# Performance work log

Hardware: AMD Instinct MI355X
Metric: run time of the kernel (lower is better)

Reference implementation:

```python
import jax, jax.numpy as jnp
import numpy as np
from jax import lax

IMG_W, IMG_H = 800.0, 320.0
NPTS = 72
N_STRIPS = NPTS - 1
MAX_LANES = 4
NUM_PRIORS = 192
STAGES = 3
B = 512
LIOU_LEN = 15.0
CLS_W, XYT_W, IOU_W, SEG_W = 2.0, 0.2, 2.0, 1.0


def smooth_l1(x):
    ax = jnp.abs(x)
    return jnp.where(ax < 1.0, 0.5 * x * x, ax - 0.5)


def pairwise_line_iou(pred_xs, tgt_xs):
    # pred_xs [P,N] pixel xs, tgt_xs [L,N]; returns [P,L]
    px1, px2 = pred_xs - LIOU_LEN, pred_xs + LIOU_LEN
    tx1, tx2 = tgt_xs - LIOU_LEN, tgt_xs + LIOU_LEN
    ovr = jnp.minimum(px2[:, None, :], tx2[None]) - jnp.maximum(px1[:, None, :], tx1[None])
    union = jnp.maximum(px2[:, None, :], tx2[None]) - jnp.minimum(px1[:, None, :], tx1[None])
    invalid = (tgt_xs < 0) | (tgt_xs >= IMG_W)
    ovr = jnp.where(invalid[None], 0.0, ovr)
    union = jnp.where(invalid[None], 0.0, union)
    return ovr.sum(-1) / (union.sum(-1) + 1e-9)


def focal_sum(logits, target):
    # kornia-style softmax focal loss (alpha=0.25, gamma=2), summed
    p = jax.nn.softmax(logits, axis=1) + 1e-8
    focal = -0.25 * (1.0 - p) ** 2 * jnp.log(p)
    oh = jax.nn.one_hot(target, 2, dtype=logits.dtype)
    return (oh * focal).sum()


def per_sample(pred, tgt):
    # pred [P, 6+N], tgt [L, 6+N]
    L = tgt.shape[0]
    f32 = pred.dtype
    valid = tgt[:, 1] == 1.0
    num_t = valid.sum()
    has_t = num_t > 0

    t_xs = tgt[:, 6:]                          # [L,N] pixel xs (-1e5 = invalid)
    pred_xs_px = pred[:, 6:] * (IMG_W - 1.0)   # [P,N]
    iou_pair = pairwise_line_iou(pred_xs_px, t_xs)  # [P,L] (grad flows for loss)

    # ---------- assignment (stop-grad, mirrors CLRNet dynamic_assign) ----------
    pd = lax.stop_gradient(pred)
    pd_xs = pd[:, 6:] * (IMG_W - 1.0)
    inv_t = (t_xs < 0) | (t_xs >= IMG_W)
    t_len = (~inv_t).sum(1).astype(f32)
    dist = jnp.where(inv_t[None], 0.0, jnp.abs(t_xs[None] - pd_xs[:, None, :])).sum(-1)
    dist = dist / (t_len[None] + 1e-9)         # [P,L]

    def norm_score(x):
        m = jnp.max(jnp.where(valid[None], x, -jnp.inf))
        m = jnp.where(has_t, m, 1.0)
        return 1.0 - x / m + 1e-2

    dist_score = norm_score(dist)
    p_xy = jnp.stack([pd[:, 2] * (IMG_H - 1.0), pd[:, 3] * (IMG_W - 1.0)], 1)
    t_xy = jnp.stack([tgt[:, 2] * (IMG_H - 1.0), tgt[:, 3]], 1)
    sd = jnp.sqrt(((p_xy[:, None] - t_xy[None]) ** 2).sum(-1))
    s_score = norm_score(sd)
    th = jnp.abs(pd[:, 4, None] - tgt[None, :, 4]) * 180.0
    th_score = norm_score(th)
    sp = jax.nn.sigmoid(pd[:, :2])
    neg = -jnp.log(1.0 - sp + 1e-12) * 0.75 * sp ** 2
    pos = -jnp.log(sp + 1e-12) * 0.25 * (1.0 - sp) ** 2
    cls_cost = pos[:, 1] - neg[:, 1]           # all gt labels are 1
    cost = -(dist_score * s_score * th_score) ** 2 * 3.0 + cls_cost[:, None]
    cost = jnp.where(valid[None], cost, jnp.inf)

    # dynamic-k (SimOTA-style)
    iou_sg = jnp.where(valid[None], jnp.maximum(lax.stop_gradient(iou_pair), 0.0), 0.0)
    topk = lax.top_k(iou_sg.T, 4)[0]           # [L,4]
    dyn_k = jnp.maximum(topk.sum(1).astype(jnp.int32), 1)
    ranks = jnp.argsort(jnp.argsort(cost, axis=0), axis=0)
    M = (ranks < dyn_k[None]) & valid[None]
    multi = M.sum(1) > 1
    argmin_col = jnp.argmin(cost, axis=1)
    Mf = M.astype(f32)
    Mf = Mf.at[:, 0].set(jnp.where(multi, 0.0, Mf[:, 0]))
    oh_min = jax.nn.one_hot(argmin_col, L, dtype=f32)
    Mf = jnp.where(multi[:, None] & (oh_min > 0), 1.0, Mf)
    n_match = Mf.sum()

    # ---------- cls loss ----------
    cls_target = (Mf.sum(1) > 0).astype(jnp.int32)
    cls_term = focal_sum(pred[:, :2], cls_target) / jnp.where(has_t, num_t.astype(f32), 1.0)

    # ---------- reg yxtl (smooth L1) ----------
    scale = jnp.array([N_STRIPS, IMG_W - 1.0, 180.0, N_STRIPS], dtype=f32)
    pred_yxtl = pred[:, 2:6] * scale           # [P,4]
    tgt3 = jnp.stack([tgt[:, 2] * N_STRIPS, tgt[:, 3], tgt[:, 4] * 180.0], 1)  # [L,3]
    pred_starts = jnp.clip(jnp.round(lax.stop_gradient(pred[:, 2]) * N_STRIPS), 0, N_STRIPS)
    tgt_starts = jnp.round(tgt[:, 2] * N_STRIPS)
    tgt_len_pair = tgt[None, :, 5] - (pred_starts[:, None] - tgt_starts[None, :])  # [P,L]
    sl = smooth_l1(pred_yxtl[:, None, :3] - tgt3[None]).sum(-1) \
       + smooth_l1(pred_yxtl[:, 3][:, None] - tgt_len_pair)
    reg_term = (Mf * sl).sum() / jnp.maximum(n_match * 4.0, 1.0)
    iou_term = (Mf * (1.0 - iou_pair)).sum() / jnp.maximum(n_match, 1.0)
    zero = jnp.zeros((), f32)
    reg_term = jnp.where(has_t, reg_term, zero)
    iou_term = jnp.where(has_t, iou_term, zero)
    return cls_term, reg_term, iou_term


def setup_inputs() -> dict:
    key = jax.random.key(0)
    ks = jax.random.split(key, 8)
    D = 6 + NPTS
    cls = jax.random.normal(ks[0], (STAGES, B, NUM_PRIORS, 2), jnp.float32)
    rest = jax.random.uniform(ks[1], (STAGES, B, NUM_PRIORS, D - 2), dtype=jnp.float32)
    predictions = jnp.concatenate([cls, rest], -1)

    valid = jax.random.uniform(ks[2], (B, MAX_LANES)) < 0.8
    start = jax.random.randint(ks[3], (B, MAX_LANES), 0, 40)
    length = jax.random.randint(ks[4], (B, MAX_LANES), 10, NPTS)
    end = jnp.minimum(start + length, NPTS)
    idx = jnp.arange(NPTS)
    inside = (idx[None, None] >= start[..., None]) & (idx[None, None] < end[..., None]) & valid[..., None]
    xs = jax.random.uniform(ks[5], (B, MAX_LANES, NPTS), minval=0.0, maxval=IMG_W - 1.0)
    xs = jnp.where(inside, xs, -1e5)
    start_x = jnp.take_along_axis(xs, start[..., None], axis=-1)[..., 0]
    theta = jax.random.uniform(ks[6], (B, MAX_LANES), minval=0.3, maxval=0.9)
    vf = valid.astype(jnp.float32)
    neg = jnp.full((B, MAX_LANES), -1e5, jnp.float32)
    targets = jnp.full((B, MAX_LANES, D), -1e5, jnp.float32)
    targets = targets.at[..., 0].set(1.0 - vf)
    targets = targets.at[..., 1].set(vf)
    targets = targets.at[..., 2].set(jnp.where(valid, start.astype(jnp.float32) / N_STRIPS, neg))
    targets = targets.at[..., 3].set(jnp.where(valid, start_x, neg))
    targets = targets.at[..., 4].set(jnp.where(valid, theta, neg))
    targets = targets.at[..., 5].set(jnp.where(valid, (end - start).astype(jnp.float32), neg))
    targets = targets.at[..., 6:].set(xs)

    seg_loss = jax.random.uniform(ks[7], (), dtype=jnp.float32)
    return {"predictions": predictions, "targets": targets, "seg_loss": seg_loss}


def reference(predictions, targets, seg_loss):
    per_batch = jax.vmap(per_sample)
    cls_l = jnp.zeros((), predictions.dtype)
    reg_l = jnp.zeros((), predictions.dtype)
    iou_l = jnp.zeros((), predictions.dtype)
    for s in range(predictions.shape[0]):  # 3 refine stages (fixed)
        c, r, i = per_batch(predictions[s], targets)
        cls_l = cls_l + c.sum()
        reg_l = reg_l + r.sum()
        iou_l = iou_l + i.sum()
    denom = targets.shape[0] * predictions.shape[0]
    cls_l = cls_l / denom
    reg_l = reg_l / denom
    iou_l = iou_l / denom
    return cls_l * CLS_W + reg_l * XYT_W + iou_l * IOU_W + seg_loss * SEG_W
```

## Files before the change

### kernel.cpp

```cpp
#include <hip/hip_runtime.h>
#include <math.h>

constexpr int kNpts   = 72;
constexpr int kPriors = 192;
constexpr int kLanes  = 4;
constexpr int kBatch  = 512;
constexpr int kStages = 3;
constexpr int kD      = 6 + kNpts;
constexpr int kBlocks = kStages * kBatch;

typedef unsigned long long u64;

__device__ __forceinline__ float smoothL1(float x) {
  float ax = fabsf(x);
  return ax < 1.0f ? 0.5f * x * x : ax - 0.5f;
}

__device__ __forceinline__ unsigned ordF(float f) {
  unsigned b = __float_as_uint(f);
  return (b & 0x80000000u) ? ~b : (b | 0x80000000u);
}

__device__ __forceinline__ void cswapA(u64& a, u64& b) {
  if (b < a) { u64 t = a; a = b; b = t; }
}
__device__ __forceinline__ void cswapD(float& a, float& b) {
  if (b > a) { float t = a; a = b; b = t; }
}
__device__ __forceinline__ u64 umin64(u64 a, u64 b) { return a < b ? a : b; }
__device__ __forceinline__ u64 umax64(u64 a, u64 b) { return a < b ? b : a; }

__global__ __launch_bounds__(192) void clr_loss_kernel(
    const float* __restrict__ pred,
    const float* __restrict__ tgt,
    float* __restrict__ partial) {
  const int blk  = blockIdx.x;
  const int b    = blk & (kBatch - 1);
  const int tid  = threadIdx.x;
  const int wav  = tid >> 6;
  const int lane = tid & 63;

  __shared__ float s_tx[kNpts][kLanes];
  __shared__ float s_m [kNpts][kLanes];
  __shared__ float s_hdr[kLanes][6];
  __shared__ float s_cost[kLanes][kPriors];
  __shared__ float s_iou[kLanes][kPriors];
  __shared__ u64   s_k3[kLanes][3];
  __shared__ int   s_dk[kLanes];
  __shared__ float s_sc[3][4];

  const float* tg = tgt + (size_t)b * kLanes * kD;
  for (int t = tid; t < kLanes * kNpts; t += 192) {
    int j = t / kNpts, k = t - j * kNpts;
    float v = tg[j * kD + 6 + k];
    s_tx[k][j] = v;
    s_m [k][j] = (v >= 0.0f && v < 800.0f) ? 1.0f : 0.0f;
  }
  if (tid < kLanes * 6) {
    int j = tid / 6, c = tid - j * 6;
    s_hdr[j][c] = tg[j * kD + c];
  }
  if (tid >= 64 && tid < 64 + kLanes) {
    int j = tid - 64;
    s_dk[j] = 1; s_k3[j][0] = 0; s_k3[j][1] = 0; s_k3[j][2] = 0;
  }

  const float*  pr   = pred + ((size_t)blk * kPriors + tid) * kD;
  const float2* rowv = (const float2*)pr;
  float2 h0 = rowv[0], h1 = rowv[1], h2 = rowv[2];
  float px[kNpts];
#pragma unroll
  for (int q = 0; q < 36; ++q) {
    float2 v = rowv[3 + q];
    px[2 * q]     = v.x * 799.0f;
    px[2 * q + 1] = v.y * 799.0f;
  }
  const float p0 = h0.x, p1 = h0.y, p2 = h1.x, p3 = h1.y, p4 = h2.x, p5 = h2.y;

  __syncthreads();

  bool validL[kLanes];
  int num_t = 0;
#pragma unroll
  for (int j = 0; j < kLanes; ++j) {
    validL[j] = (s_hdr[j][1] == 1.0f);
    num_t += validL[j] ? 1 : 0;
  }
  const bool has_t = num_t > 0;

  float ds[kLanes] = {0.0f, 0.0f, 0.0f, 0.0f};
  {
    const float4* tx4 = (const float4*)&s_tx[0][0];
    const float4* m4  = (const float4*)&s_m[0][0];
#pragma unroll
    for (int k = 0; k < kNpts; ++k) {
      float4 t = tx4[k];
      float4 m = m4[k];
      float p = px[k];
      ds[0] = fmaf(m.x, fabsf(t.x - p), ds[0]);
      ds[1] = fmaf(m.y, fabsf(t.y - p), ds[1]);
      ds[2] = fmaf(m.z, fabsf(t.z - p), ds[2]);
      ds[3] = fmaf(m.w, fabsf(t.w - p), ds[3]);
    }
  }

  float iou[kLanes], dist[kLanes], sd[kLanes], th[kLanes];
  float md = -INFINITY, ms = -INFINITY, mt = -INFINITY;
  const float py = p2 * 319.0f, pxc = p3 * 799.0f;
#pragma unroll
  for (int j = 0; j < kLanes; ++j) {
    float tlen = validL[j] ? s_hdr[j][5] : 0.0f;
    float ovr = fmaf(tlen, 30.0f, -ds[j]);
    float uni = fmaf(tlen, 30.0f,  ds[j]) + 1e-9f;
    iou[j]  = ovr / uni;
    dist[j] = ds[j] / (tlen + 1e-9f);
    float dy = py - s_hdr[j][2] * 319.0f;
    float dx = pxc - s_hdr[j][3];
    sd[j] = sqrtf(dy * dy + dx * dx);
    th[j] = fabsf(p4 - s_hdr[j][4]) * 180.0f;
    if (validL[j]) {
      md = fmaxf(md, dist[j]);
      ms = fmaxf(ms, sd[j]);
      mt = fmaxf(mt, th[j]);
    }
  }

#pragma unroll
  for (int off = 32; off; off >>= 1) {
    md = fmaxf(md, __shfl_down(md, off, 64));
    ms = fmaxf(ms, __shfl_down(ms, off, 64));
    mt = fmaxf(mt, __shfl_down(mt, off, 64));
  }
  if (lane == 0) { s_sc[wav][0] = md; s_sc[wav][1] = ms; s_sc[wav][2] = mt; }
  __syncthreads();
  md = fmaxf(fmaxf(s_sc[0][0], s_sc[1][0]), s_sc[2][0]);
  ms = fmaxf(fmaxf(s_sc[0][1], s_sc[1][1]), s_sc[2][1]);
  mt = fmaxf(fmaxf(s_sc[0][2], s_sc[1][2]), s_sc[2][2]);
  if (!has_t) { md = 1.0f; ms = 1.0f; mt = 1.0f; }

  const float sp1  = 1.0f / (1.0f + expf(-p1));
  const float neg1 = -logf(1.0f - sp1 + 1e-12f) * 0.75f * sp1 * sp1;
  const float om1  = 1.0f - sp1;
  const float pos1 = -logf(sp1 + 1e-12f) * 0.25f * om1 * om1;
  const float cls_cost = pos1 - neg1;

  float costr[kLanes];
#pragma unroll
  for (int j = 0; j < kLanes; ++j) {
    s_iou[j][tid] = validL[j] ? fmaxf(iou[j], 0.0f) : 0.0f;
    float c;
    if (validL[j]) {
      float a = (1.0f - dist[j] / md) + 0.01f;
      float s = (1.0f - sd[j] / ms) + 0.01f;
      float t = (1.0f - th[j] / mt) + 0.01f;
      float g = a * s * t;
      c = cls_cost - g * g * 3.0f;
    } else {
      c = INFINITY;
    }
    costr[j] = c;
    s_cost[j][tid] = c;
  }
  __syncthreads();

  for (int t = wav; t < 8; t += 3) {
    const int j = t & 3;
    if (!validL[j]) continue;
    if (t < 4) {
      float c0 = s_cost[j][lane], c1 = s_cost[j][lane + 64], c2 = s_cost[j][lane + 128];
      u64 k0 = ((u64)ordF(c0) << 32) | (unsigned)lane;
      u64 k1 = ((u64)ordF(c1) << 32) | (unsigned)(lane + 64);
      u64 k2 = ((u64)ordF(c2) << 32) | (unsigned)(lane + 128);
      cswapA(k0, k1); cswapA(k0, k2); cswapA(k1, k2);
#pragma unroll
      for (int off = 1; off < 64; off <<= 1) {
        u64 b0 = __shfl_xor(k0, off), b1 = __shfl_xor(k1, off), b2 = __shfl_xor(k2, off);
        u64 x0 = umin64(k0, b0), y0 = umax64(k0, b0);
        u64 x1 = umin64(k1, b1);
        u64 mc = umin64(k2, b2);
        k0 = x0;
        k2 = umin64(umax64(y0, x1), mc);
        k1 = umin64(y0, x1);
      }
      if (lane == 0) { s_k3[j][0] = k0; s_k3[j][1] = k1; s_k3[j][2] = k2; }
    } else {
      float t0 = s_iou[j][lane], t1 = s_iou[j][lane + 64], t2 = s_iou[j][lane + 128];
      float t3 = -1.0f;
      cswapD(t0, t1); cswapD(t0, t2); cswapD(t1, t2);
#pragma unroll
      for (int off = 1; off < 64; off <<= 1) {
        float b0 = __shfl_xor(t0, off), b1 = __shfl_xor(t1, off);
        float b2 = __shfl_xor(t2, off), b3 = __shfl_xor(t3, off);
        float m0 = fmaxf(t0, b3), m1 = fmaxf(t1, b2);
        float m2 = fmaxf(t2, b1), m3 = fmaxf(t3, b0);
        cswapD(m0, m2); cswapD(m1, m3); cswapD(m0, m1); cswapD(m2, m3);
        t0 = m0; t1 = m1; t2 = m2; t3 = m3;
      }
      if (lane == 0) {
        float s = ((t0 + t1) + t2) + t3;
        int dk = (int)s;
        if (dk < 1) dk = 1;
        if (dk > 3) dk = 3;
        s_dk[j] = dk;
      }
    }
  }
  __syncthreads();

  int Mi[kLanes];
  int msum = 0;
#pragma unroll
  for (int j = 0; j < kLanes; ++j) {
    u64 myk = ((u64)ordF(costr[j]) << 32) | (unsigned)tid;
    Mi[j] = (validL[j] && myk <= s_k3[j][s_dk[j] - 1]) ? 1 : 0;
    msum += Mi[j];
  }

  float amin = costr[0];
  int aidx = 0;
#pragma unroll
  for (int j = 1; j < kLanes; ++j)
    if (costr[j] < amin) { amin = costr[j]; aidx = j; }

  float Mf[kLanes];
#pragma unroll
  for (int j = 0; j < kLanes; ++j) Mf[j] = (float)Mi[j];
  if (msum > 1) {
    Mf[0] = 0.0f;
    Mf[aidx] = 1.0f;
  }

  const float mfsum = Mf[0] + Mf[1] + Mf[2] + Mf[3];
  const int cls_t = (mfsum > 0.0f) ? 1 : 0;

  const float mx = fmaxf(p0, p1);
  const float e0 = expf(p0 - mx), e1 = expf(p1 - mx);
  const float inv = 1.0f / (e0 + e1);
  const float q = (cls_t ? e1 : e0) * inv + 1e-8f;
  const float omq = 1.0f - q;
  const float focal = -0.25f * omq * omq * logf(q);

  const float pred_start = fminf(fmaxf(rintf(p2 * 71.0f), 0.0f), 71.0f);
  const float py0 = p2 * 71.0f, py1 = p3 * 799.0f, py2t = p4 * 180.0f, py3 = p5 * 71.0f;
  float regc = 0.0f, iouc = 0.0f;
#pragma unroll
  for (int j = 0; j < kLanes; ++j) {
    if (Mf[j] > 0.0f) {
      float t30 = s_hdr[j][2] * 71.0f;
      float t31 = s_hdr[j][3];
      float t32 = s_hdr[j][4] * 180.0f;
      float tstart = rintf(s_hdr[j][2] * 71.0f);
      float tlp = s_hdr[j][5] - (pred_start - tstart);
      regc += smoothL1(py0 - t30) + smoothL1(py1 - t31) + smoothL1(py2t - t32)
            + smoothL1(py3 - tlp);
      iouc += 1.0f - iou[j];
    }
  }

  float v0 = mfsum, v1 = focal, v2 = regc, v3 = iouc;
#pragma unroll
  for (int off = 32; off; off >>= 1) {
    v0 += __shfl_down(v0, off, 64);
    v1 += __shfl_down(v1, off, 64);
    v2 += __shfl_down(v2, off, 64);
    v3 += __shfl_down(v3, off, 64);
  }
  __syncthreads();
  if (lane == 0) {
    s_sc[wav][0] = v0; s_sc[wav][1] = v1; s_sc[wav][2] = v2; s_sc[wav][3] = v3;
  }
  __syncthreads();

  if (tid == 0) {
    float nm      = s_sc[0][0] + s_sc[1][0] + s_sc[2][0];
    float cls_sum = s_sc[0][1] + s_sc[1][1] + s_sc[2][1];
    float reg_sum = s_sc[0][2] + s_sc[1][2] + s_sc[2][2];
    float iou_sum = s_sc[0][3] + s_sc[1][3] + s_sc[2][3];

    float cls_term = cls_sum / (has_t ? (float)num_t : 1.0f);
    float reg_term = has_t ? reg_sum / fmaxf(nm * 4.0f, 1.0f) : 0.0f;
    float iou_term = has_t ? iou_sum / fmaxf(nm, 1.0f) : 0.0f;

    partial[blk] = 2.0f * cls_term + 0.2f * reg_term + 2.0f * iou_term;
  }
}

__global__ __launch_bounds__(256) void clr_reduce(
    const float* __restrict__ partial,
    const float* __restrict__ seg,
    float* __restrict__ out) {
  const int tid  = threadIdx.x;
  const int wav  = tid >> 6;
  const int lane = tid & 63;
  __shared__ float sc[4];

  float s = 0.0f;
#pragma unroll
  for (int i = 0; i < kBlocks / 256; ++i) s += partial[tid + 256 * i];
#pragma unroll
  for (int off = 32; off; off >>= 1) s += __shfl_down(s, off, 64);
  if (lane == 0) sc[wav] = s;
  __syncthreads();
  if (tid == 0) {
    float tot = ((sc[0] + sc[1]) + sc[2]) + sc[3];
    out[0] = tot * (1.0f / (float)kBlocks) + seg[0];
  }
}

extern "C" void kernel_launch(void* const* d_in, const int* in_sizes, int n_in,
                              void* d_out, int out_size, void* d_ws, size_t ws_size,
                              hipStream_t stream) {
  const float* pred = (const float*)d_in[0];
  const float* tgt  = (const float*)d_in[1];
  const float* seg  = (const float*)d_in[2];
  float* out     = (float*)d_out;
  float* partial = (float*)d_ws;

  clr_loss_kernel<<<kBlocks, 192, 0, stream>>>(pred, tgt, partial);
  clr_reduce<<<1, 256, 0, stream>>>(partial, seg, out);
}
```

Baseline: 147.2 us.

## Load prediction rows with aligned float4 reads and interleave loads with distance accumulation

Each thread now reads its 78-float prediction row as 16-byte-aligned float4 vectors, shifting the base back by 8 bytes on odd threads, instead of 39 float2 loads. The target and mask tables in shared memory get two zero pad rows at each end so the shifted indices stay in bounds and the pad points add nothing. The global loads are spread through the unrolled distance loop so memory latency overlaps with arithmetic. Launch bounds now ask for 5 blocks per CU to limit register use, and the header load moves to other threads, at the cost of more complex indexing.

```diff
diff --git a/kernel.cpp b/kernel.cpp
--- a/kernel.cpp
+++ b/kernel.cpp
@@ -8,6 +8,7 @@
 constexpr int kStages = 3;
 constexpr int kD      = 6 + kNpts;
 constexpr int kBlocks = kStages * kBatch;
+constexpr int kTRows  = kNpts + 4;
 
 typedef unsigned long long u64;
 
@@ -30,7 +31,19 @@
 __device__ __forceinline__ u64 umin64(u64 a, u64 b) { return a < b ? a : b; }
 __device__ __forceinline__ u64 umax64(u64 a, u64 b) { return a < b ? b : a; }
 
-__global__ __launch_bounds__(192) void clr_loss_kernel(
+#define DS_STEP(val, I) {                                     \
+    const float p_ = (val) * 799.0f;                          \
+    const float4 tt = *(const float4*)(txb + 4 * ((I) - 4));  \
+    const float4 mm = *(const float4*)(mbp + 4 * ((I) - 4));  \
+    ds0 = fmaf(mm.x, fabsf(tt.x - p_), ds0);                  \
+    ds1 = fmaf(mm.y, fabsf(tt.y - p_), ds1);                  \
+    ds2 = fmaf(mm.z, fabsf(tt.z - p_), ds2);                  \
+    ds3 = fmaf(mm.w, fabsf(tt.w - p_), ds3); }
+
+#define DS_G(v, I0) DS_STEP((v).x, (I0)) DS_STEP((v).y, (I0) + 1) \
+                    DS_STEP((v).z, (I0) + 2) DS_STEP((v).w, (I0) + 3)
+
+__global__ __launch_bounds__(192, 5) void clr_loss_kernel(
     const float* __restrict__ pred,
     const float* __restrict__ tgt,
     float* __restrict__ partial) {
@@ -40,8 +53,8 @@
   const int wav  = tid >> 6;
   const int lane = tid & 63;
 
-  __shared__ float s_tx[kNpts][kLanes];
-  __shared__ float s_m [kNpts][kLanes];
+  __shared__ __align__(16) float s_tx[kTRows][kLanes];
+  __shared__ __align__(16) float s_m [kTRows][kLanes];
   __shared__ float s_hdr[kLanes][6];
   __shared__ float s_cost[kLanes][kPriors];
   __shared__ float s_iou[kLanes][kPriors];
@@ -53,11 +66,18 @@
   for (int t = tid; t < kLanes * kNpts; t += 192) {
     int j = t / kNpts, k = t - j * kNpts;
     float v = tg[j * kD + 6 + k];
-    s_tx[k][j] = v;
-    s_m [k][j] = (v >= 0.0f && v < 800.0f) ? 1.0f : 0.0f;
-  }
-  if (tid < kLanes * 6) {
-    int j = tid / 6, c = tid - j * 6;
+    s_tx[k + 2][j] = v;
+    s_m [k + 2][j] = (v >= 0.0f && v < 800.0f) ? 1.0f : 0.0f;
+  }
+  if (tid < 16) {
+    int row = (tid >> 3) * 74 + ((tid >> 2) & 1);
+    int j = tid & 3;
+    s_tx[row][j] = 0.0f;
+    s_m [row][j] = 0.0f;
+  }
+  if (tid >= 32 && tid < 32 + kLanes * 6) {
+    int u = tid - 32;
+    int j = u / 6, c = u - j * 6;
     s_hdr[j][c] = tg[j * kD + c];
   }
   if (tid >= 64 && tid < 64 + kLanes) {
@@ -65,17 +85,11 @@
     s_dk[j] = 1; s_k3[j][0] = 0; s_k3[j][1] = 0; s_k3[j][2] = 0;
   }
 
-  const float*  pr   = pred + ((size_t)blk * kPriors + tid) * kD;
-  const float2* rowv = (const float2*)pr;
-  float2 h0 = rowv[0], h1 = rowv[1], h2 = rowv[2];
-  float px[kNpts];
-#pragma unroll
-  for (int q = 0; q < 36; ++q) {
-    float2 v = rowv[3 + q];
-    px[2 * q]     = v.x * 799.0f;
-    px[2 * q + 1] = v.y * 799.0f;
-  }
-  const float p0 = h0.x, p1 = h0.y, p2 = h1.x, p3 = h1.y, p4 = h2.x, p5 = h2.y;
+  const float* rowp = pred + ((size_t)blk * kPriors + tid) * kD;
+  const int o = tid & 1;
+  const float4* aw = (const float4*)((const char*)rowp - (o << 3));
+  float4 hc0 = aw[0], hc1 = aw[1];
+  float4 g0 = aw[2], g1 = aw[3], g2 = aw[4], g3 = aw[5], g4 = aw[6], g5 = aw[7];
 
   __syncthreads();
 
@@ -88,21 +102,35 @@
   }
   const bool has_t = num_t > 0;
 
-  float ds[kLanes] = {0.0f, 0.0f, 0.0f, 0.0f};
-  {
-    const float4* tx4 = (const float4*)&s_tx[0][0];
-    const float4* m4  = (const float4*)&s_m[0][0];
-#pragma unroll
-    for (int k = 0; k < kNpts; ++k) {
-      float4 t = tx4[k];
-      float4 m = m4[k];
-      float p = px[k];
-      ds[0] = fmaf(m.x, fabsf(t.x - p), ds[0]);
-      ds[1] = fmaf(m.y, fabsf(t.y - p), ds[1]);
-      ds[2] = fmaf(m.z, fabsf(t.z - p), ds[2]);
-      ds[3] = fmaf(m.w, fabsf(t.w - p), ds[3]);
-    }
-  }
+  const float p0 = o ? hc0.z : hc0.x;
+  const float p1 = o ? hc0.w : hc0.y;
+  const float p2 = o ? hc1.x : hc0.z;
+  const float p3 = o ? hc1.y : hc0.w;
+  const float p4 = o ? hc1.z : hc1.x;
+  const float p5 = o ? hc1.w : hc1.y;
+
+  const float* txb = &s_tx[0][0] - (o << 3);
+  const float* mbp = &s_m [0][0] - (o << 3);
+  float ds0 = 0.0f, ds1 = 0.0f, ds2 = 0.0f, ds3 = 0.0f;
+
+  DS_STEP(hc1.z, 6) DS_STEP(hc1.w, 7)
+  float4 g6 = aw[8],  g7 = aw[9];
+  DS_G(g0, 8)  DS_G(g1, 12)
+  float4 g8 = aw[10], g9 = aw[11];
+  DS_G(g2, 16) DS_G(g3, 20)
+  float4 gA = aw[12], gB = aw[13];
+  DS_G(g4, 24) DS_G(g5, 28)
+  float4 gC = aw[14], gD = aw[15];
+  DS_G(g6, 32) DS_G(g7, 36)
+  float4 gE = aw[16], gF = aw[17];
+  DS_G(g8, 40) DS_G(g9, 44)
+  float4 gG = aw[18], gH = aw[19];
+  DS_G(gA, 48) DS_G(gB, 52)
+  DS_G(gC, 56) DS_G(gD, 60)
+  DS_G(gE, 64) DS_G(gF, 68)
+  DS_G(gG, 72) DS_G(gH, 76)
+
+  float ds[kLanes] = {ds0, ds1, ds2, ds3};
 
   float iou[kLanes], dist[kLanes], sd[kLanes], th[kLanes];
   float md = -INFINITY, ms = -INFINITY, mt = -INFINITY;
@@ -285,6 +313,9 @@
   }
 }
 
+#undef DS_STEP
+#undef DS_G
+
 __global__ __launch_bounds__(256) void clr_reduce(
     const float* __restrict__ partial,
     const float* __restrict__ seg,
```

Measured after the change: 155.8 us. 1.06x slower.

## Prepack target lanes and stream them via scalar loads instead of LDS

Applied to the files above, without the earlier changes.

A new prep kernel interleaves each sample's target xs and validity masks into a packed [k][tx4,m4] layout in workspace. The main kernel then reads that packed data with inline-asm s_load_dwordx16 scalar loads into SGPRs, while software-pipelining the per-thread prediction xs loads three groups ahead. This removes the LDS staging loop, the 72-float px register array and the LDS reads in the distance accumulation. In exchange it adds an extra kernel launch, hand-written asm with a full lgkmcnt wait per group, and a fallback to the old LDS kernel when the workspace is too small.

```diff
diff --git a/kernel.cpp b/kernel.cpp
--- a/kernel.cpp
+++ b/kernel.cpp
@@ -8,8 +8,11 @@
 constexpr int kStages = 3;
 constexpr int kD      = 6 + kNpts;
 constexpr int kBlocks = kStages * kBatch;
+constexpr int kPackOffset = 2048;
+constexpr int kPackFloats = kBatch * kNpts * 8;
 
 typedef unsigned long long u64;
+typedef float fv16 __attribute__((ext_vector_type(16)));
 
 __device__ __forceinline__ float smoothL1(float x) {
   float ax = fabsf(x);
@@ -30,18 +33,55 @@
 __device__ __forceinline__ u64 umin64(u64 a, u64 b) { return a < b ? a : b; }
 __device__ __forceinline__ u64 umax64(u64 a, u64 b) { return a < b ? b : a; }
 
-__global__ __launch_bounds__(192) void clr_loss_kernel(
+__global__ __launch_bounds__(256) void clr_prep(
+    const float* __restrict__ tgt, float* __restrict__ pack) {
+  int i = blockIdx.x * 256 + threadIdx.x;
+  if (i >= kBatch * kNpts) return;
+  int b = i / kNpts, k = i - b * kNpts;
+  const float* tg = tgt + (size_t)b * kLanes * kD + 6 + k;
+  float v0 = tg[0 * kD], v1 = tg[1 * kD], v2 = tg[2 * kD], v3 = tg[3 * kD];
+  float4 tx = make_float4(v0, v1, v2, v3);
+  float4 m  = make_float4((v0 >= 0.0f && v0 < 800.0f) ? 1.0f : 0.0f,
+                          (v1 >= 0.0f && v1 < 800.0f) ? 1.0f : 0.0f,
+                          (v2 >= 0.0f && v2 < 800.0f) ? 1.0f : 0.0f,
+                          (v3 >= 0.0f && v3 < 800.0f) ? 1.0f : 0.0f);
+  float4* o = (float4*)(pack + (size_t)i * 8);
+  o[0] = tx;
+  o[1] = m;
+}
+
+#define SGRP(OFF0, OFF1, SA, SB)                                          \
+  asm volatile("s_load_dwordx16 %0, %2, %3\n\t"                           \
+               "s_load_dwordx16 %1, %2, %4\n\t"                           \
+               "s_waitcnt lgkmcnt(0)"                                     \
+               : "=s"(SA), "=s"(SB)                                       \
+               : "s"(pka), "n"(OFF0), "n"(OFF1));
+
+#define KQUAD(SV, E0, PXV)                                                \
+  { const float px_ = (PXV) * 799.0f;                                     \
+    ds0 = fmaf(SV[(E0) + 4], fabsf(SV[(E0) + 0] - px_), ds0);             \
+    ds1 = fmaf(SV[(E0) + 5], fabsf(SV[(E0) + 1] - px_), ds1);             \
+    ds2 = fmaf(SV[(E0) + 6], fabsf(SV[(E0) + 2] - px_), ds2);             \
+    ds3 = fmaf(SV[(E0) + 7], fabsf(SV[(E0) + 3] - px_), ds3); }
+
+#define GRP(G, CA, CB, PA, PB, DOPF)                                      \
+  { fv16 SA_, SB_;                                                        \
+    SGRP(128 * (G), 128 * (G) + 64, SA_, SB_)                             \
+    if (DOPF) { PA = rowv[7 + 2 * (G)]; PB = rowv[8 + 2 * (G)]; }         \
+    KQUAD(SA_, 0, CA.x) KQUAD(SA_, 8, CA.y)                               \
+    KQUAD(SB_, 0, CB.x) KQUAD(SB_, 8, CB.y) }
+
+__global__ __launch_bounds__(192, 4) void clr_loss_smem(
     const float* __restrict__ pred,
     const float* __restrict__ tgt,
-    float* __restrict__ partial) {
+    float* __restrict__ partial,
+    const float* __restrict__ pack) {
   const int blk  = blockIdx.x;
   const int b    = blk & (kBatch - 1);
   const int tid  = threadIdx.x;
   const int wav  = tid >> 6;
   const int lane = tid & 63;
 
-  __shared__ float s_tx[kNpts][kLanes];
-  __shared__ float s_m [kNpts][kLanes];
   __shared__ float s_hdr[kLanes][6];
   __shared__ float s_cost[kLanes][kPriors];
   __shared__ float s_iou[kLanes][kPriors];
@@ -50,12 +90,6 @@
   __shared__ float s_sc[3][4];
 
   const float* tg = tgt + (size_t)b * kLanes * kD;
-  for (int t = tid; t < kLanes * kNpts; t += 192) {
-    int j = t / kNpts, k = t - j * kNpts;
-    float v = tg[j * kD + 6 + k];
-    s_tx[k][j] = v;
-    s_m [k][j] = (v >= 0.0f && v < 800.0f) ? 1.0f : 0.0f;
-  }
   if (tid < kLanes * 6) {
     int j = tid / 6, c = tid - j * 6;
     s_hdr[j][c] = tg[j * kD + c];
@@ -68,14 +102,35 @@
   const float*  pr   = pred + ((size_t)blk * kPriors + tid) * kD;
   const float2* rowv = (const float2*)pr;
   float2 h0 = rowv[0], h1 = rowv[1], h2 = rowv[2];
-  float px[kNpts];
-#pragma unroll
-  for (int q = 0; q < 36; ++q) {
-    float2 v = rowv[3 + q];
-    px[2 * q]     = v.x * 799.0f;
-    px[2 * q + 1] = v.y * 799.0f;
-  }
   const float p0 = h0.x, p1 = h0.y, p2 = h1.x, p3 = h1.y, p4 = h2.x, p5 = h2.y;
+
+  const unsigned long long pka =
+      (unsigned long long)(const void*)(pack + (size_t)b * (kNpts * 8));
+  float ds0 = 0.0f, ds1 = 0.0f, ds2 = 0.0f, ds3 = 0.0f;
+  {
+    float2 q0a = rowv[3], q0b = rowv[4];
+    float2 q1a = rowv[5], q1b = rowv[6];
+    float2 q2a, q2b;
+    GRP(0,  q0a, q0b, q2a, q2b, true)
+    GRP(1,  q1a, q1b, q0a, q0b, true)
+    GRP(2,  q2a, q2b, q1a, q1b, true)
+    GRP(3,  q0a, q0b, q2a, q2b, true)
+    GRP(4,  q1a, q1b, q0a, q0b, true)
+    GRP(5,  q2a, q2b, q1a, q1b, true)
+    GRP(6,  q0a, q0b, q2a, q2b, true)
+    GRP(7,  q1a, q1b, q0a, q0b, true)
+    GRP(8,  q2a, q2b, q1a, q1b, true)
+    GRP(9,  q0a, q0b, q2a, q2b, true)
+    GRP(10, q1a, q1b, q0a, q0b, true)
+    GRP(11, q2a, q2b, q1a, q1b, true)
+    GRP(12, q0a, q0b, q2a, q2b, true)
+    GRP(13, q1a, q1b, q0a, q0b, true)
+    GRP(14, q2a, q2b, q1a, q1b, true)
+    GRP(15, q0a, q0b, q2a, q2b, true)
+    GRP(16, q1a, q1b, q2a, q2b, false)
+    GRP(17, q2a, q2b, q2a, q2b, false)
+  }
+  float ds[kLanes] = {ds0, ds1, ds2, ds3};
 
   __syncthreads();
 
@@ -87,22 +142,6 @@
     num_t += validL[j] ? 1 : 0;
   }
   const bool has_t = num_t > 0;
-
-  float ds[kLanes] = {0.0f, 0.0f, 0.0f, 0.0f};
-  {
-    const float4* tx4 = (const float4*)&s_tx[0][0];
-    const float4* m4  = (const float4*)&s_m[0][0];
-#pragma unroll
-    for (int k = 0; k < kNpts; ++k) {
-      float4 t = tx4[k];
-      float4 m = m4[k];
-      float p = px[k];
-      ds[0] = fmaf(m.x, fabsf(t.x - p), ds[0]);
-      ds[1] = fmaf(m.y, fabsf(t.y - p), ds[1]);
-      ds[2] = fmaf(m.z, fabsf(t.z - p), ds[2]);
-      ds[3] = fmaf(m.w, fabsf(t.w - p), ds[3]);
-    }
-  }
 
   float iou[kLanes], dist[kLanes], sd[kLanes], th[kLanes];
   float md = -INFINITY, ms = -INFINITY, mt = -INFINITY;
@@ -285,6 +324,265 @@
   }
 }
 
+#undef GRP
+#undef KQUAD
+#undef SGRP
+
+__global__ __launch_bounds__(192) void clr_loss_lds(
+    const float* __restrict__ pred,
+    const float* __restrict__ tgt,
+    float* __restrict__ partial) {
+  const int blk  = blockIdx.x;
+  const int b    = blk & (kBatch - 1);
+  const int tid  = threadIdx.x;
+  const int wav  = tid >> 6;
+  const int lane = tid & 63;
+
+  __shared__ float s_tx[kNpts][kLanes];
+  __shared__ float s_m [kNpts][kLanes];
+  __shared__ float s_hdr[kLanes][6];
+  __shared__ float s_cost[kLanes][kPriors];
+  __shared__ float s_iou[kLanes][kPriors];
+  __shared__ u64   s_k3[kLanes][3];
+  __shared__ int   s_dk[kLanes];
+  __shared__ float s_sc[3][4];
+
+  const float* tg = tgt + (size_t)b * kLanes * kD;
+  for (int t = tid; t < kLanes * kNpts; t += 192) {
+    int j = t / kNpts, k = t - j * kNpts;
+    float v = tg[j * kD + 6 + k];
+    s_tx[k][j] = v;
+    s_m [k][j] = (v >= 0.0f && v < 800.0f) ? 1.0f : 0.0f;
+  }
+  if (tid < kLanes * 6) {
+    int j = tid / 6, c = tid - j * 6;
+    s_hdr[j][c] = tg[j * kD + c];
+  }
+  if (tid >= 64 && tid < 64 + kLanes) {
+    int j = tid - 64;
+    s_dk[j] = 1; s_k3[j][0] = 0; s_k3[j][1] = 0; s_k3[j][2] = 0;
+  }
+
+  const float*  pr   = pred + ((size_t)blk * kPriors + tid) * kD;
+  const float2* rowv = (const float2*)pr;
+  float2 h0 = rowv[0], h1 = rowv[1], h2 = rowv[2];
+  float px[kNpts];
+#pragma unroll
+  for (int q = 0; q < 36; ++q) {
+    float2 v = rowv[3 + q];
+    px[2 * q]     = v.x * 799.0f;
+    px[2 * q + 1] = v.y * 799.0f;
+  }
+  const float p0 = h0.x, p1 = h0.y, p2 = h1.x, p3 = h1.y, p4 = h2.x, p5 = h2.y;
+
+  __syncthreads();
+
+  bool validL[kLanes];
+  int num_t = 0;
+#pragma unroll
+  for (int j = 0; j < kLanes; ++j) {
+    validL[j] = (s_hdr[j][1] == 1.0f);
+    num_t += validL[j] ? 1 : 0;
+  }
+  const bool has_t = num_t > 0;
+
+  float ds[kLanes] = {0.0f, 0.0f, 0.0f, 0.0f};
+  {
+    const float4* tx4 = (const float4*)&s_tx[0][0];
+    const float4* m4  = (const float4*)&s_m[0][0];
+#pragma unroll
+    for (int k = 0; k < kNpts; ++k) {
+      float4 t = tx4[k];
+      float4 m = m4[k];
+      float p = px[k];
+      ds[0] = fmaf(m.x, fabsf(t.x - p), ds[0]);
+      ds[1] = fmaf(m.y, fabsf(t.y - p), ds[1]);
+      ds[2] = fmaf(m.z, fabsf(t.z - p), ds[2]);
+      ds[3] = fmaf(m.w, fabsf(t.w - p), ds[3]);
+    }
+  }
+
+  float iou[kLanes], dist[kLanes], sd[kLanes], th[kLanes];
+  float md = -INFINITY, ms = -INFINITY, mt = -INFINITY;
+  const float py = p2 * 319.0f, pxc = p3 * 799.0f;
+#pragma unroll
+  for (int j = 0; j < kLanes; ++j) {
+    float tlen = validL[j] ? s_hdr[j][5] : 0.0f;
+    float ovr = fmaf(tlen, 30.0f, -ds[j]);
+    float uni = fmaf(tlen, 30.0f,  ds[j]) + 1e-9f;
+    iou[j]  = ovr / uni;
+    dist[j] = ds[j] / (tlen + 1e-9f);
+    float dy = py - s_hdr[j][2] * 319.0f;
+    float dx = pxc - s_hdr[j][3];
+    sd[j] = sqrtf(dy * dy + dx * dx);
+    th[j] = fabsf(p4 - s_hdr[j][4]) * 180.0f;
+    if (validL[j]) {
+      md = fmaxf(md, dist[j]);
+      ms = fmaxf(ms, sd[j]);
+      mt = fmaxf(mt, th[j]);
+    }
+  }
+
+#pragma unroll
+  for (int off = 32; off; off >>= 1) {
+    md = fmaxf(md, __shfl_down(md, off, 64));
+    ms = fmaxf(ms, __shfl_down(ms, off, 64));
+    mt = fmaxf(mt, __shfl_down(mt, off, 64));
+  }
+  if (lane == 0) { s_sc[wav][0] = md; s_sc[wav][1] = ms; s_sc[wav][2] = mt; }
+  __syncthreads();
+  md = fmaxf(fmaxf(s_sc[0][0], s_sc[1][0]), s_sc[2][0]);
+  ms = fmaxf(fmaxf(s_sc[0][1], s_sc[1][1]), s_sc[2][1]);
+  mt = fmaxf(fmaxf(s_sc[0][2], s_sc[1][2]), s_sc[2][2]);
+  if (!has_t) { md = 1.0f; ms = 1.0f; mt = 1.0f; }
+
+  const float sp1  = 1.0f / (1.0f + expf(-p1));
+  const float neg1 = -logf(1.0f - sp1 + 1e-12f) * 0.75f * sp1 * sp1;
+  const float om1  = 1.0f - sp1;
+  const float pos1 = -logf(sp1 + 1e-12f) * 0.25f * om1 * om1;
+  const float cls_cost = pos1 - neg1;
+
+  float costr[kLanes];
+#pragma unroll
+  for (int j = 0; j < kLanes; ++j) {
+    s_iou[j][tid] = validL[j] ? fmaxf(iou[j], 0.0f) : 0.0f;
+    float c;
+    if (validL[j]) {
+      float a = (1.0f - dist[j] / md) + 0.01f;
+      float s = (1.0f - sd[j] / ms) + 0.01f;
+      float t = (1.0f - th[j] / mt) + 0.01f;
+      float g = a * s * t;
+      c = cls_cost - g * g * 3.0f;
+    } else {
+      c = INFINITY;
+    }
+    costr[j] = c;
+    s_cost[j][tid] = c;
+  }
+  __syncthreads();
+
+  for (int t = wav; t < 8; t += 3) {
+    const int j = t & 3;
+    if (!validL[j]) continue;
+    if (t < 4) {
+      float c0 = s_cost[j][lane], c1 = s_cost[j][lane + 64], c2 = s_cost[j][lane + 128];
+      u64 k0 = ((u64)ordF(c0) << 32) | (unsigned)lane;
+      u64 k1 = ((u64)ordF(c1) << 32) | (unsigned)(lane + 64);
+      u64 k2 = ((u64)ordF(c2) << 32) | (unsigned)(lane + 128);
+      cswapA(k0, k1); cswapA(k0, k2); cswapA(k1, k2);
+#pragma unroll
+      for (int off = 1; off < 64; off <<= 1) {
+        u64 b0 = __shfl_xor(k0, off), b1 = __shfl_xor(k1, off), b2 = __shfl_xor(k2, off);
+        u64 x0 = umin64(k0, b0), y0 = umax64(k0, b0);
+        u64 x1 = umin64(k1, b1);
+        u64 mc = umin64(k2, b2);
+        k0 = x0;
+        k2 = umin64(umax64(y0, x1), mc);
+        k1 = umin64(y0, x1);
+      }
+      if (lane == 0) { s_k3[j][0] = k0; s_k3[j][1] = k1; s_k3[j][2] = k2; }
+    } else {
+      float t0 = s_iou[j][lane], t1 = s_iou[j][lane + 64], t2 = s_iou[j][lane + 128];
+      float t3 = -1.0f;
+      cswapD(t0, t1); cswapD(t0, t2); cswapD(t1, t2);
+#pragma unroll
+      for (int off = 1; off < 64; off <<= 1) {
+        float b0 = __shfl_xor(t0, off), b1 = __shfl_xor(t1, off);
+        float b2 = __shfl_xor(t2, off), b3 = __shfl_xor(t3, off);
+        float m0 = fmaxf(t0, b3), m1 = fmaxf(t1, b2);
+        float m2 = fmaxf(t2, b1), m3 = fmaxf(t3, b0);
+        cswapD(m0, m2); cswapD(m1, m3); cswapD(m0, m1); cswapD(m2, m3);
+        t0 = m0; t1 = m1; t2 = m2; t3 = m3;
+      }
+      if (lane == 0) {
+        float s = ((t0 + t1) + t2) + t3;
+        int dk = (int)s;
+        if (dk < 1) dk = 1;
+        if (dk > 3) dk = 3;
+        s_dk[j] = dk;
+      }
+    }
+  }
+  __syncthreads();
+
+  int Mi[kLanes];
+  int msum = 0;
+#pragma unroll
+  for (int j = 0; j < kLanes; ++j) {
+    u64 myk = ((u64)ordF(costr[j]) << 32) | (unsigned)tid;
+    Mi[j] = (validL[j] && myk <= s_k3[j][s_dk[j] - 1]) ? 1 : 0;
+    msum += Mi[j];
+  }
+
+  float amin = costr[0];
+  int aidx = 0;
+#pragma unroll
+  for (int j = 1; j < kLanes; ++j)
+    if (costr[j] < amin) { amin = costr[j]; aidx = j; }
+
+  float Mf[kLanes];
+#pragma unroll
+  for (int j = 0; j < kLanes; ++j) Mf[j] = (float)Mi[j];
+  if (msum > 1) {
+    Mf[0] = 0.0f;
+    Mf[aidx] = 1.0f;
+  }
+
+  const float mfsum = Mf[0] + Mf[1] + Mf[2] + Mf[3];
+  const int cls_t = (mfsum > 0.0f) ? 1 : 0;
+
+  const float mx = fmaxf(p0, p1);
+  const float e0 = expf(p0 - mx), e1 = expf(p1 - mx);
+  const float inv = 1.0f / (e0 + e1);
+  const float q = (cls_t ? e1 : e0) * inv + 1e-8f;
+  const float omq = 1.0f - q;
+  const float focal = -0.25f * omq * omq * logf(q);
+
+  const float pred_start = fminf(fmaxf(rintf(p2 * 71.0f), 0.0f), 71.0f);
+  const float py0 = p2 * 71.0f, py1 = p3 * 799.0f, py2t = p4 * 180.0f, py3 = p5 * 71.0f;
+  float regc = 0.0f, iouc = 0.0f;
+#pragma unroll
+  for (int j = 0; j < kLanes; ++j) {
+    if (Mf[j] > 0.0f) {
+      float t30 = s_hdr[j][2] * 71.0f;
+      float t31 = s_hdr[j][3];
+      float t32 = s_hdr[j][4] * 180.0f;
+      float tstart = rintf(s_hdr[j][2] * 71.0f);
+      float tlp = s_hdr[j][5] - (pred_start - tstart);
+      regc += smoothL1(py0 - t30) + smoothL1(py1 - t31) + smoothL1(py2t - t32)
+            + smoothL1(py3 - tlp);
+      iouc += 1.0f - iou[j];
+    }
+  }
+
+  float v0 = mfsum, v1 = focal, v2 = regc, v3 = iouc;
+#pragma unroll
+  for (int off = 32; off; off >>= 1) {
+    v0 += __shfl_down(v0, off, 64);
+    v1 += __shfl_down(v1, off, 64);
+    v2 += __shfl_down(v2, off, 64);
+    v3 += __shfl_down(v3, off, 64);
+  }
+  __syncthreads();
+  if (lane == 0) {
+    s_sc[wav][0] = v0; s_sc[wav][1] = v1; s_sc[wav][2] = v2; s_sc[wav][3] = v3;
+  }
+  __syncthreads();
+
+  if (tid == 0) {
+    float nm      = s_sc[0][0] + s_sc[1][0] + s_sc[2][0];
+    float cls_sum = s_sc[0][1] + s_sc[1][1] + s_sc[2][1];
+    float reg_sum = s_sc[0][2] + s_sc[1][2] + s_sc[2][2];
+    float iou_sum = s_sc[0][3] + s_sc[1][3] + s_sc[2][3];
+
+    float cls_term = cls_sum / (has_t ? (float)num_t : 1.0f);
+    float reg_term = has_t ? reg_sum / fmaxf(nm * 4.0f, 1.0f) : 0.0f;
+    float iou_term = has_t ? iou_sum / fmaxf(nm, 1.0f) : 0.0f;
+
+    partial[blk] = 2.0f * cls_term + 0.2f * reg_term + 2.0f * iou_term;
+  }
+}
+
 __global__ __launch_bounds__(256) void clr_reduce(
     const float* __restrict__ partial,
     const float* __restrict__ seg,
@@ -316,6 +614,13 @@
   float* out     = (float*)d_out;
   float* partial = (float*)d_ws;
 
-  clr_loss_kernel<<<kBlocks, 192, 0, stream>>>(pred, tgt, partial);
+  const size_t need = (size_t)(kPackOffset + kPackFloats) * sizeof(float);
+  if (ws_size >= need) {
+    float* pack = (float*)d_ws + kPackOffset;
+    clr_prep<<<(kBatch * kNpts + 255) / 256, 256, 0, stream>>>(tgt, pack);
+    clr_loss_smem<<<kBlocks, 192, 0, stream>>>(pred, tgt, partial, pack);
+  } else {
+    clr_loss_lds<<<kBlocks, 192, 0, stream>>>(pred, tgt, partial);
+  }
   clr_reduce<<<1, 256, 0, stream>>>(partial, seg, out);
 }
```

New measurement: 171.7 us. 16.7% more time.
